# Kernel tuning notes

Hardware: AMD Instinct MI355X
Metric: run time of the kernel (lower is better)

The kernel has to match this reference:

```python
import jax, jax.numpy as jnp
import numpy as np


def setup_inputs() -> dict:
    key = jax.random.key(0)
    k0, k1, k2, k3 = jax.random.split(key, 4)
    B, C, L1, L2, U = 256, 128, 32, 32, 128
    return {
        "inputs": jax.random.normal(k0, (B, C, L1, L2), jnp.float32),
        "W": jax.random.normal(k1, (C + 3 * U, 7 * U), jnp.float32) * 0.05,
        "Umat": jax.random.normal(k2, (3 * U, U), jnp.float32) * 0.05,
        "bias": jnp.zeros((8 * U,), jnp.float32),
        "w_ij": jax.random.normal(k3, (C, U), jnp.float32) * 0.05,
    }


def _hard_sigmoid(x):
    # keras hard_sigmoid
    return jnp.clip(0.2 * x + 0.5, 0.0, 1.0)


def _spatial_gru(inputs, W, Umat, bias, w_ij):
    B, C, L1, L2 = inputs.shape
    U = w_ij.shape[1]
    wr, wz = W[:, : 3 * U], W[:, 3 * U : 7 * U]
    br, bz, b_ij = bias[: 3 * U], bias[3 * U : 7 * U], bias[7 * U :]
    s = jnp.transpose(inputs, (2, 3, 0, 1))  # (L1, L2, B, C)
    h0 = jnp.zeros((B, U), inputs.dtype)

    def cell(h_left, inp):
        h_diag, h_top, s_ij = inp  # each (B, U) / (B, C)
        # q = [h_top, h_left, h_diag, s_ij]  (B, 3U + C)
        q = jnp.concatenate([h_top, h_left, h_diag, s_ij], axis=1)
        r = _hard_sigmoid(q @ wr + br)                      # (B, 3U)
        z = q @ wz + bz                                     # (B, 4U)
        # softmax across the 4 gates per unit (softmax_by_row)
        zg = jax.nn.softmax(z.reshape(B, 4, U), axis=1)
        zi, zl, zt, zd = zg[:, 0], zg[:, 1], zg[:, 2], zg[:, 3]
        hij_ = jnp.tanh(
            s_ij @ w_ij + b_ij
            + (r * jnp.concatenate([h_left, h_top, h_diag], axis=1)) @ Umat
        )
        hij = zl * h_left + zt * h_top + zd * h_diag + zi * hij_
        return hij, hij

    def row(prev_row, s_row):
        # prev_row: (L2+1, B, U) hidden states of row above, boundary h0 at col 0
        # h_diag_j = prev_row[j], h_top_j = prev_row[j+1]
        _, row_h = jax.lax.scan(cell, h0, (prev_row[:-1], prev_row[1:], s_row))
        new_row = jnp.concatenate([h0[None], row_h], axis=0)  # (L2+1, B, U)
        return new_row, None

    init_row = jnp.zeros((L2 + 1, B, U), inputs.dtype)
    last_row, _ = jax.lax.scan(row, init_row, s)
    return last_row[-1]  # h at bottom-right cell, (B, U)


def reference(inputs, W, Umat, bias, w_ij):
    return _spatial_gru(inputs, W, Umat, bias, w_ij)
```

## Files before the change

### kernel.cpp

```cpp
#include <hip/hip_runtime.h>
#include <hip/hip_bf16.h>

typedef _Float16 f16x8 __attribute__((ext_vector_type(8)));
typedef float f32x4 __attribute__((ext_vector_type(4)));

#define BATCH 256
#define UD 128
#define K1 512
#define LDA 520
#define LDA2 392
#define CELLSZ (BATCH*UD)
#define RINGSZ (32*CELLSZ)

__global__ void k_reorder(const float* __restrict__ in, _Float16* __restrict__ X){
  int b = blockIdx.x, i = blockIdx.y;
  __shared__ float tile[128][33];
  int tid = threadIdx.x;
#pragma unroll
  for (int r=0;r<16;++r){
    int c = r*8 + (tid>>5), j = tid&31;
    tile[c][j] = in[(((size_t)b*128 + c)*32 + i)*32 + j];
  }
  __syncthreads();
#pragma unroll
  for (int r=0;r<16;++r){
    int j = r*2 + (tid>>7), c = tid&127;
    X[((size_t)(i*32 + j)*256 + b)*128 + c] = (_Float16)tile[c][j];
  }
}

__global__ void k_prep(const float* __restrict__ W,
                       const float* __restrict__ Um,
                       const float* __restrict__ wij,
                       _Float16* __restrict__ WT, _Float16* __restrict__ B2T){
  int idx = blockIdx.x*256 + threadIdx.x;
  if (idx < 896*512){
    int n = idx >> 9, k = idx & 511;
    WT[idx] = (_Float16)W[k*896 + n];
  }
  if (idx < 128*512){
    int n = idx >> 9, k = idx & 511;
    float v = (k < 384) ? Um[k*128 + n] : wij[(k-384)*128 + n];
    B2T[idx] = (_Float16)v;
  }
}

__global__ void k_out(const float* __restrict__ ring, float* __restrict__ out){
  int t = blockIdx.x*256 + threadIdx.x;
  out[t] = ring[(size_t)2*RINGSZ + (size_t)31*CELLSZ + t];
}

__global__ __launch_bounds__(256, 1) void k_diag(
    int d,
    const _Float16* __restrict__ X,
    float* __restrict__ ring,
    const _Float16* __restrict__ WT,
    const _Float16* __restrict__ B2T,
    const float* __restrict__ bias)
{
  __shared__ __align__(16) _Float16 Al[32*LDA];
  __shared__ __align__(16) _Float16 A2l[32*LDA2];

  const int i0 = (d > 31) ? (d - 31) : 0;
  const int i = i0 + blockIdx.x;
  const int j = d - i;
  const int bs = blockIdx.y * 32;

  const int tid  = threadIdx.x;
  const int wave = tid >> 6;
  const int lane = tid & 63;
  const int l15  = lane & 15;
  const int quad = lane >> 4;

  const bool hasT = (i >= 1);
  const bool hasL = (j >= 1);
  const bool hasD = hasT && hasL;

  const float* rm1 = ring + (size_t)((d+2)%3)*RINGSZ;
  const float* rm2 = ring + (size_t)((d+1)%3)*RINGSZ;
  float*       rw  = ring + (size_t)(d%3)*RINGSZ;

  const float* hTop  = rm1 + (size_t)(i-1)*CELLSZ;
  const float* hLeft = rm1 + (size_t)i*CELLSZ;
  const float* hDiag = rm2 + (size_t)(i-1)*CELLSZ;
  float*       hOut  = rw  + (size_t)i*CELLSZ;
  const _Float16* Xc = X + (size_t)(i*32 + j)*CELLSZ;

  {
    const float* srcs[3];
    srcs[0] = hasT ? hTop : nullptr;
    srcs[1] = hasL ? hLeft : nullptr;
    srcs[2] = hasD ? hDiag : nullptr;
#pragma unroll
    for (int r=0;r<3;++r){
      const float* src = srcs[r];
      if (src){
        for (int v = tid; v < 1024; v += 256){
          int m = v >> 5, kc = (v & 31) << 2;
          float4 f = *(const float4*)(src + (size_t)(bs+m)*UD + kc);
          union { _Float16 h[4]; ushort4 u; } p;
          p.h[0]=(_Float16)f.x; p.h[1]=(_Float16)f.y;
          p.h[2]=(_Float16)f.z; p.h[3]=(_Float16)f.w;
          *(ushort4*)&Al[m*LDA + r*128 + kc] = p.u;
        }
      } else {
        for (int v = tid; v < 1024; v += 256){
          int m = v >> 5, kc = (v & 31) << 2;
          *(ushort4*)&Al[m*LDA + r*128 + kc] = make_ushort4(0,0,0,0);
        }
      }
    }
    for (int v = tid; v < 512; v += 256){
      int m = v >> 4, kc = (v & 15) << 3;
      *(uint4*)&Al[m*LDA + 384 + kc] = *(const uint4*)(Xc + (size_t)(bs+m)*UD + kc);
    }
  }
  __syncthreads();

  f32x4 acc[2][14];
#pragma unroll
  for (int a=0;a<2;++a)
#pragma unroll
    for (int t=0;t<14;++t) acc[a][t] = (f32x4){0.f,0.f,0.f,0.f};

  {
    const _Float16* bptr[14];
#pragma unroll
    for (int t=0;t<14;++t){
      const int n = (t<6) ? (wave*96 + t*16)
                          : (384 + ((t-6)>>1)*128 + wave*32 + ((t-6)&1)*16);
      bptr[t] = WT + (size_t)(n + l15)*K1 + quad*8;
    }
    f16x8 bcur[14], bnxt[14];
#pragma unroll
    for (int t=0;t<14;++t) bcur[t] = *(const f16x8*)(bptr[t]);
#pragma unroll
    for (int ks=0; ks<16; ++ks){
      const int kb = ks*32 + quad*8;
      if (ks < 15){
#pragma unroll
        for (int t=0;t<14;++t) bnxt[t] = *(const f16x8*)(bptr[t] + (ks+1)*32);
      }
      f16x8 a0 = *(const f16x8*)&Al[l15*LDA + kb];
      f16x8 a1 = *(const f16x8*)&Al[(16+l15)*LDA + kb];
#pragma unroll
      for (int t=0;t<14;++t){
        acc[0][t] = __builtin_amdgcn_mfma_f32_16x16x32_f16(a0, bcur[t], acc[0][t], 0,0,0);
        acc[1][t] = __builtin_amdgcn_mfma_f32_16x16x32_f16(a1, bcur[t], acc[1][t], 0,0,0);
      }
#pragma unroll
      for (int t=0;t<14;++t) bcur[t] = bnxt[t];
    }
  }

#pragma unroll
  for (int mt=0;mt<2;++mt)
#pragma unroll
    for (int t=0;t<6;++t){
      const int col = wave*96 + t*16 + l15;
      const float br = bias[col];
      const int hcol = (col < 128) ? (128 + col) : ((col < 256) ? (col - 128) : col);
#pragma unroll
      for (int rg=0;rg<4;++rg){
        const int m = mt*16 + quad*4 + rg;
        float r = 0.2f*(acc[mt][t][rg] + br) + 0.5f;
        r = fminf(fmaxf(r, 0.f), 1.f);
        float h = (float)Al[m*LDA + hcol];
        A2l[m*LDA2 + col] = (_Float16)(r*h);
      }
    }
  __syncthreads();

  f32x4 acc2[2][2];
#pragma unroll
  for (int a=0;a<2;++a){ acc2[a][0]=(f32x4){0.f,0.f,0.f,0.f}; acc2[a][1]=(f32x4){0.f,0.f,0.f,0.f}; }
  {
    const _Float16* b2ptr[2];
#pragma unroll
    for (int s=0;s<2;++s) b2ptr[s] = B2T + (size_t)(wave*32 + s*16 + l15)*K1 + quad*8;
    f16x8 b2cur[2], b2nxt[2];
#pragma unroll
    for (int s=0;s<2;++s) b2cur[s] = *(const f16x8*)(b2ptr[s]);
#pragma unroll
    for (int ks=0; ks<16; ++ks){
      const int kb = ks*32 + quad*8;
      if (ks < 15){
#pragma unroll
        for (int s=0;s<2;++s) b2nxt[s] = *(const f16x8*)(b2ptr[s] + (ks+1)*32);
      }
      f16x8 a0, a1;
      if (ks < 12){
        a0 = *(const f16x8*)&A2l[l15*LDA2 + kb];
        a1 = *(const f16x8*)&A2l[(16+l15)*LDA2 + kb];
      } else {
        a0 = *(const f16x8*)&Al[l15*LDA + kb];
        a1 = *(const f16x8*)&Al[(16+l15)*LDA + kb];
      }
#pragma unroll
      for (int s=0;s<2;++s){
        acc2[0][s] = __builtin_amdgcn_mfma_f32_16x16x32_f16(a0, b2cur[s], acc2[0][s], 0,0,0);
        acc2[1][s] = __builtin_amdgcn_mfma_f32_16x16x32_f16(a1, b2cur[s], acc2[1][s], 0,0,0);
      }
#pragma unroll
      for (int s=0;s<2;++s) b2cur[s] = b2nxt[s];
    }
  }

#pragma unroll
  for (int mt=0;mt<2;++mt)
#pragma unroll
    for (int s=0;s<2;++s){
      const int u = wave*32 + s*16 + l15;
      const float bz0 = bias[384 + 0*128 + u];
      const float bz1 = bias[384 + 1*128 + u];
      const float bz2 = bias[384 + 2*128 + u];
      const float bz3 = bias[384 + 3*128 + u];
      const float bij = bias[896 + u];
#pragma unroll
      for (int rg=0;rg<4;++rg){
        const int m = mt*16 + quad*4 + rg;
        const size_t row = (size_t)(bs+m)*UD + u;
        float z0 = acc[mt][6 + 0 + s][rg] + bz0;
        float z1 = acc[mt][6 + 2 + s][rg] + bz1;
        float z2 = acc[mt][6 + 4 + s][rg] + bz2;
        float z3 = acc[mt][6 + 6 + s][rg] + bz3;
        float mx = fmaxf(fmaxf(z0,z1), fmaxf(z2,z3));
        float e0 = __expf(z0-mx), e1 = __expf(z1-mx), e2 = __expf(z2-mx), e3 = __expf(z3-mx);
        float inv = 1.f/(e0+e1+e2+e3);
        float hl = hasL ? hLeft[row] : 0.f;
        float ht = hasT ? hTop[row]  : 0.f;
        float hd = hasD ? hDiag[row] : 0.f;
        float cand = tanhf(acc2[mt][s][rg] + bij);
        hOut[row] = (e1*hl + e2*ht + e3*hd + e0*cand)*inv;
      }
    }
}

extern "C" void kernel_launch(void* const* d_in, const int* in_sizes, int n_in,
                              void* d_out, int out_size, void* d_ws, size_t ws_size,
                              hipStream_t stream){
  const float* inp  = (const float*)d_in[0];
  const float* W    = (const float*)d_in[1];
  const float* Um   = (const float*)d_in[2];
  const float* bias = (const float*)d_in[3];
  const float* wij  = (const float*)d_in[4];
  float* out = (float*)d_out;

  char* ws = (char*)d_ws;
  _Float16* WT   = (_Float16*)(ws);
  _Float16* B2T  = (_Float16*)(ws + 917504);
  _Float16* X    = (_Float16*)(ws + 1048576);
  float*    ring = (float*)   (ws + 68157440);

  k_reorder<<<dim3(256,32),256,0,stream>>>(inp, X);
  k_prep<<<1792,256,0,stream>>>(W, Um, wij, WT, B2T);
  for (int d=0; d<63; ++d){
    int ilo = (d>31)?(d-31):0, ihi = (d<31)?d:31;
    int nc = ihi - ilo + 1;
    k_diag<<<dim3(nc,8),256,0,stream>>>(d, X, ring, WT, B2T, bias);
  }
  k_out<<<128,256,0,stream>>>(ring, out);
}
```

Before: 2.778 ms.

## Replace per-diagonal launches with persistent wavefront kernel using per-cell flags

```diff
diff --git a/kernel.cpp b/kernel.cpp
--- a/kernel.cpp
+++ b/kernel.cpp
@@ -10,7 +10,11 @@
 #define LDA 520
 #define LDA2 392
 #define CELLSZ (BATCH*UD)
-#define RINGSZ (32*CELLSZ)
+
+#define WS_B2T  917504
+#define WS_X    1048576
+#define WS_H    68157440ull
+#define WS_FLAG 202375168ull
 
 __global__ void k_reorder(const float* __restrict__ in, _Float16* __restrict__ X){
   int b = blockIdx.x, i = blockIdx.y;
@@ -32,7 +36,8 @@
 __global__ void k_prep(const float* __restrict__ W,
                        const float* __restrict__ Um,
                        const float* __restrict__ wij,
-                       _Float16* __restrict__ WT, _Float16* __restrict__ B2T){
+                       _Float16* __restrict__ WT, _Float16* __restrict__ B2T,
+                       unsigned* __restrict__ flags){
   int idx = blockIdx.x*256 + threadIdx.x;
   if (idx < 896*512){
     int n = idx >> 9, k = idx & 511;
@@ -43,28 +48,63 @@
     float v = (k < 384) ? Um[k*128 + n] : wij[(k-384)*128 + n];
     B2T[idx] = (_Float16)v;
   }
-}
-
-__global__ void k_out(const float* __restrict__ ring, float* __restrict__ out){
+  if (idx < 1024*8) flags[idx] = 0;
+}
+
+__global__ void k_out(const float* __restrict__ H, float* __restrict__ out){
   int t = blockIdx.x*256 + threadIdx.x;
-  out[t] = ring[(size_t)2*RINGSZ + (size_t)31*CELLSZ + t];
-}
-
-__global__ __launch_bounds__(256, 1) void k_diag(
-    int d,
+  out[t] = H[(size_t)1023*CELLSZ + t];
+}
+
+template<int T0>
+__device__ __forceinline__ void gemm1_pass(const _Float16* Al,
+    const _Float16* __restrict__ WT, int wave, int l15, int quad,
+    f32x4 (&acc)[2][7])
+{
+  const _Float16* bptr[7];
+#pragma unroll
+  for (int t=0;t<7;++t){
+    const int tt = T0 + t;
+    const int n = (tt<6) ? (wave*96 + tt*16)
+                         : (384 + ((tt-6)>>1)*128 + wave*32 + ((tt-6)&1)*16);
+    bptr[t] = WT + (size_t)(n + l15)*K1 + quad*8;
+  }
+  f16x8 bcur[7], bnxt[7];
+#pragma unroll
+  for (int t=0;t<7;++t) bcur[t] = *(const f16x8*)(bptr[t]);
+#pragma unroll
+  for (int ks=0; ks<16; ++ks){
+    const int kb = ks*32 + quad*8;
+    if (ks < 15){
+#pragma unroll
+      for (int t=0;t<7;++t) bnxt[t] = *(const f16x8*)(bptr[t] + (ks+1)*32);
+    }
+    f16x8 a0 = *(const f16x8*)&Al[l15*LDA + kb];
+    f16x8 a1 = *(const f16x8*)&Al[(16+l15)*LDA + kb];
+#pragma unroll
+    for (int t=0;t<7;++t){
+      acc[0][t] = __builtin_amdgcn_mfma_f32_16x16x32_f16(a0, bcur[t], acc[0][t], 0,0,0);
+      acc[1][t] = __builtin_amdgcn_mfma_f32_16x16x32_f16(a1, bcur[t], acc[1][t], 0,0,0);
+    }
+#pragma unroll
+    for (int t=0;t<7;++t) bcur[t] = bnxt[t];
+  }
+}
+
+__global__ __launch_bounds__(256, 2) void k_sweep(
     const _Float16* __restrict__ X,
-    float* __restrict__ ring,
+    float* __restrict__ H,
     const _Float16* __restrict__ WT,
     const _Float16* __restrict__ B2T,
-    const float* __restrict__ bias)
+    const float* __restrict__ bias,
+    unsigned* __restrict__ flags)
 {
   __shared__ __align__(16) _Float16 Al[32*LDA];
   __shared__ __align__(16) _Float16 A2l[32*LDA2];
 
-  const int i0 = (d > 31) ? (d - 31) : 0;
-  const int i = i0 + blockIdx.x;
-  const int j = d - i;
-  const int bs = blockIdx.y * 32;
+  const int c     = blockIdx.x;
+  const int strip = blockIdx.y;
+  const int bs    = strip*32;
 
   const int tid  = threadIdx.x;
   const int wave = tid >> 6;
@@ -72,168 +112,173 @@
   const int l15  = lane & 15;
   const int quad = lane >> 4;
 
-  const bool hasT = (i >= 1);
-  const bool hasL = (j >= 1);
-  const bool hasD = hasT && hasL;
-
-  const float* rm1 = ring + (size_t)((d+2)%3)*RINGSZ;
-  const float* rm2 = ring + (size_t)((d+1)%3)*RINGSZ;
-  float*       rw  = ring + (size_t)(d%3)*RINGSZ;
-
-  const float* hTop  = rm1 + (size_t)(i-1)*CELLSZ;
-  const float* hLeft = rm1 + (size_t)i*CELLSZ;
-  const float* hDiag = rm2 + (size_t)(i-1)*CELLSZ;
-  float*       hOut  = rw  + (size_t)i*CELLSZ;
-  const _Float16* Xc = X + (size_t)(i*32 + j)*CELLSZ;
-
-  {
-    const float* srcs[3];
-    srcs[0] = hasT ? hTop : nullptr;
-    srcs[1] = hasL ? hLeft : nullptr;
-    srcs[2] = hasD ? hDiag : nullptr;
-#pragma unroll
-    for (int r=0;r<3;++r){
-      const float* src = srcs[r];
-      if (src){
-        for (int v = tid; v < 1024; v += 256){
-          int m = v >> 5, kc = (v & 31) << 2;
-          float4 f = *(const float4*)(src + (size_t)(bs+m)*UD + kc);
-          union { _Float16 h[4]; ushort4 u; } p;
-          p.h[0]=(_Float16)f.x; p.h[1]=(_Float16)f.y;
-          p.h[2]=(_Float16)f.z; p.h[3]=(_Float16)f.w;
-          *(ushort4*)&Al[m*LDA + r*128 + kc] = p.u;
-        }
-      } else {
-        for (int v = tid; v < 1024; v += 256){
-          int m = v >> 5, kc = (v & 31) << 2;
-          *(ushort4*)&Al[m*LDA + r*128 + kc] = make_ushort4(0,0,0,0);
-        }
-      }
-    }
+  for (int d = c; d <= 62 - c; ++d){
+    const int i0 = (d > 31) ? (d - 31) : 0;
+    const int i  = i0 + c;
+    const int j  = d - i;
+    const bool hasT = (i >= 1);
+    const bool hasL = (j >= 1);
+    const bool hasD = hasT && hasL;
+
+    const int cell = i*32 + j;
+    const _Float16* Xc   = X + (size_t)cell*CELLSZ;
+    float*       hOut    = H + (size_t)cell*CELLSZ;
+    const float* hTop    = H + (size_t)(cell-32)*CELLSZ;
+    const float* hLeft   = H + (size_t)(cell-1)*CELLSZ;
+    const float* hDiag   = H + (size_t)(cell-33)*CELLSZ;
+
     for (int v = tid; v < 512; v += 256){
       int m = v >> 4, kc = (v & 15) << 3;
       *(uint4*)&Al[m*LDA + 384 + kc] = *(const uint4*)(Xc + (size_t)(bs+m)*UD + kc);
     }
-  }
-  __syncthreads();
-
-  f32x4 acc[2][14];
-#pragma unroll
-  for (int a=0;a<2;++a)
-#pragma unroll
-    for (int t=0;t<14;++t) acc[a][t] = (f32x4){0.f,0.f,0.f,0.f};
-
-  {
-    const _Float16* bptr[14];
-#pragma unroll
-    for (int t=0;t<14;++t){
-      const int n = (t<6) ? (wave*96 + t*16)
-                          : (384 + ((t-6)>>1)*128 + wave*32 + ((t-6)&1)*16);
-      bptr[t] = WT + (size_t)(n + l15)*K1 + quad*8;
-    }
-    f16x8 bcur[14], bnxt[14];
-#pragma unroll
-    for (int t=0;t<14;++t) bcur[t] = *(const f16x8*)(bptr[t]);
-#pragma unroll
-    for (int ks=0; ks<16; ++ks){
-      const int kb = ks*32 + quad*8;
-      if (ks < 15){
-#pragma unroll
-        for (int t=0;t<14;++t) bnxt[t] = *(const f16x8*)(bptr[t] + (ks+1)*32);
-      }
-      f16x8 a0 = *(const f16x8*)&Al[l15*LDA + kb];
-      f16x8 a1 = *(const f16x8*)&Al[(16+l15)*LDA + kb];
-#pragma unroll
-      for (int t=0;t<14;++t){
-        acc[0][t] = __builtin_amdgcn_mfma_f32_16x16x32_f16(a0, bcur[t], acc[0][t], 0,0,0);
-        acc[1][t] = __builtin_amdgcn_mfma_f32_16x16x32_f16(a1, bcur[t], acc[1][t], 0,0,0);
-      }
-#pragma unroll
-      for (int t=0;t<14;++t) bcur[t] = bnxt[t];
-    }
-  }
-
-#pragma unroll
-  for (int mt=0;mt<2;++mt)
-#pragma unroll
-    for (int t=0;t<6;++t){
-      const int col = wave*96 + t*16 + l15;
-      const float br = bias[col];
-      const int hcol = (col < 128) ? (128 + col) : ((col < 256) ? (col - 128) : col);
-#pragma unroll
-      for (int rg=0;rg<4;++rg){
-        const int m = mt*16 + quad*4 + rg;
-        float r = 0.2f*(acc[mt][t][rg] + br) + 0.5f;
-        r = fminf(fmaxf(r, 0.f), 1.f);
-        float h = (float)Al[m*LDA + hcol];
-        A2l[m*LDA2 + col] = (_Float16)(r*h);
-      }
-    }
-  __syncthreads();
-
-  f32x4 acc2[2][2];
-#pragma unroll
-  for (int a=0;a<2;++a){ acc2[a][0]=(f32x4){0.f,0.f,0.f,0.f}; acc2[a][1]=(f32x4){0.f,0.f,0.f,0.f}; }
-  {
-    const _Float16* b2ptr[2];
-#pragma unroll
-    for (int s=0;s<2;++s) b2ptr[s] = B2T + (size_t)(wave*32 + s*16 + l15)*K1 + quad*8;
-    f16x8 b2cur[2], b2nxt[2];
-#pragma unroll
-    for (int s=0;s<2;++s) b2cur[s] = *(const f16x8*)(b2ptr[s]);
-#pragma unroll
-    for (int ks=0; ks<16; ++ks){
-      const int kb = ks*32 + quad*8;
-      if (ks < 15){
-#pragma unroll
-        for (int s=0;s<2;++s) b2nxt[s] = *(const f16x8*)(b2ptr[s] + (ks+1)*32);
-      }
-      f16x8 a0, a1;
-      if (ks < 12){
-        a0 = *(const f16x8*)&A2l[l15*LDA2 + kb];
-        a1 = *(const f16x8*)&A2l[(16+l15)*LDA2 + kb];
-      } else {
-        a0 = *(const f16x8*)&Al[l15*LDA + kb];
-        a1 = *(const f16x8*)&Al[(16+l15)*LDA + kb];
-      }
+    if (!hasT || !hasL){
+#pragma unroll
+      for (int r=0;r<3;++r){
+        const bool present = (r==0) ? hasT : ((r==1) ? hasL : hasD);
+        if (!present){
+          for (int v = tid; v < 1024; v += 256){
+            int m = v >> 5, kc = (v & 31) << 2;
+            *(ushort4*)&Al[m*LDA + r*128 + kc] = make_ushort4(0,0,0,0);
+          }
+        }
+      }
+    }
+
+    if (tid < 3){
+      const unsigned* f = nullptr;
+      if (tid==0 && hasT) f = &flags[(size_t)(cell-32)*8 + strip];
+      if (tid==1 && hasL) f = &flags[(size_t)(cell-1)*8 + strip];
+      if (tid==2 && hasD) f = &flags[(size_t)(cell-33)*8 + strip];
+      if (f){
+        while (__hip_atomic_load(f, __ATOMIC_RELAXED, __HIP_MEMORY_SCOPE_AGENT) == 0)
+          __builtin_amdgcn_s_sleep(1);
+      }
+    }
+    __syncthreads();
+
+    {
+      const float* srcs[3];
+      srcs[0] = hasT ? hTop : nullptr;
+      srcs[1] = hasL ? hLeft : nullptr;
+      srcs[2] = hasD ? hDiag : nullptr;
+#pragma unroll
+      for (int r=0;r<3;++r){
+        const float* src = srcs[r];
+        if (src){
+          for (int v = tid; v < 1024; v += 256){
+            int m = v >> 5, kc = (v & 31) << 2;
+            float4 f4 = *(const float4*)(src + (size_t)(bs+m)*UD + kc);
+            union { _Float16 h[4]; ushort4 u; } p;
+            p.h[0]=(_Float16)f4.x; p.h[1]=(_Float16)f4.y;
+            p.h[2]=(_Float16)f4.z; p.h[3]=(_Float16)f4.w;
+            *(ushort4*)&Al[m*LDA + r*128 + kc] = p.u;
+          }
+        }
+      }
+    }
+    __syncthreads();
+
+    f32x4 accA[2][7];
+#pragma unroll
+    for (int a=0;a<2;++a)
+#pragma unroll
+      for (int t=0;t<7;++t) accA[a][t] = (f32x4){0.f,0.f,0.f,0.f};
+    gemm1_pass<0>(Al, WT, wave, l15, quad, accA);
+
+#pragma unroll
+    for (int mt=0;mt<2;++mt)
+#pragma unroll
+      for (int t=0;t<6;++t){
+        const int col = wave*96 + t*16 + l15;
+        const float br = bias[col];
+        const int hcol = (col < 128) ? (128 + col) : ((col < 256) ? (col - 128) : col);
+#pragma unroll
+        for (int rg=0;rg<4;++rg){
+          const int m = mt*16 + quad*4 + rg;
+          float r = 0.2f*(accA[mt][t][rg] + br) + 0.5f;
+          r = fminf(fmaxf(r, 0.f), 1.f);
+          float h = (float)Al[m*LDA + hcol];
+          A2l[m*LDA2 + col] = (_Float16)(r*h);
+        }
+      }
+
+    f32x4 accB[2][7];
+#pragma unroll
+    for (int a=0;a<2;++a)
+#pragma unroll
+      for (int t=0;t<7;++t) accB[a][t] = (f32x4){0.f,0.f,0.f,0.f};
+    gemm1_pass<7>(Al, WT, wave, l15, quad, accB);
+    __syncthreads();
+
+    f32x4 acc2[2][2];
+#pragma unroll
+    for (int a=0;a<2;++a){ acc2[a][0]=(f32x4){0.f,0.f,0.f,0.f}; acc2[a][1]=(f32x4){0.f,0.f,0.f,0.f}; }
+    {
+      const _Float16* b2ptr[2];
+#pragma unroll
+      for (int s=0;s<2;++s) b2ptr[s] = B2T + (size_t)(wave*32 + s*16 + l15)*K1 + quad*8;
+      f16x8 b2cur[2], b2nxt[2];
+#pragma unroll
+      for (int s=0;s<2;++s) b2cur[s] = *(const f16x8*)(b2ptr[s]);
+#pragma unroll
+      for (int ks=0; ks<16; ++ks){
+        const int kb = ks*32 + quad*8;
+        if (ks < 15){
+#pragma unroll
+          for (int s=0;s<2;++s) b2nxt[s] = *(const f16x8*)(b2ptr[s] + (ks+1)*32);
+        }
+        f16x8 a0, a1;
+        if (ks < 12){
+          a0 = *(const f16x8*)&A2l[l15*LDA2 + kb];
+          a1 = *(const f16x8*)&A2l[(16+l15)*LDA2 + kb];
+        } else {
+          a0 = *(const f16x8*)&Al[l15*LDA + kb];
+          a1 = *(const f16x8*)&Al[(16+l15)*LDA + kb];
+        }
+#pragma unroll
+        for (int s=0;s<2;++s){
+          acc2[0][s] = __builtin_amdgcn_mfma_f32_16x16x32_f16(a0, b2cur[s], acc2[0][s], 0,0,0);
+          acc2[1][s] = __builtin_amdgcn_mfma_f32_16x16x32_f16(a1, b2cur[s], acc2[1][s], 0,0,0);
+        }
+#pragma unroll
+        for (int s=0;s<2;++s) b2cur[s] = b2nxt[s];
+      }
+    }
+
+#pragma unroll
+    for (int mt=0;mt<2;++mt)
 #pragma unroll
       for (int s=0;s<2;++s){
-        acc2[0][s] = __builtin_amdgcn_mfma_f32_16x16x32_f16(a0, b2cur[s], acc2[0][s], 0,0,0);
-        acc2[1][s] = __builtin_amdgcn_mfma_f32_16x16x32_f16(a1, b2cur[s], acc2[1][s], 0,0,0);
-      }
-#pragma unroll
-      for (int s=0;s<2;++s) b2cur[s] = b2nxt[s];
-    }
-  }
-
-#pragma unroll
-  for (int mt=0;mt<2;++mt)
-#pragma unroll
-    for (int s=0;s<2;++s){
-      const int u = wave*32 + s*16 + l15;
-      const float bz0 = bias[384 + 0*128 + u];
-      const float bz1 = bias[384 + 1*128 + u];
-      const float bz2 = bias[384 + 2*128 + u];
-      const float bz3 = bias[384 + 3*128 + u];
-      const float bij = bias[896 + u];
-#pragma unroll
-      for (int rg=0;rg<4;++rg){
-        const int m = mt*16 + quad*4 + rg;
-        const size_t row = (size_t)(bs+m)*UD + u;
-        float z0 = acc[mt][6 + 0 + s][rg] + bz0;
-        float z1 = acc[mt][6 + 2 + s][rg] + bz1;
-        float z2 = acc[mt][6 + 4 + s][rg] + bz2;
-        float z3 = acc[mt][6 + 6 + s][rg] + bz3;
-        float mx = fmaxf(fmaxf(z0,z1), fmaxf(z2,z3));
-        float e0 = __expf(z0-mx), e1 = __expf(z1-mx), e2 = __expf(z2-mx), e3 = __expf(z3-mx);
-        float inv = 1.f/(e0+e1+e2+e3);
-        float hl = hasL ? hLeft[row] : 0.f;
-        float ht = hasT ? hTop[row]  : 0.f;
-        float hd = hasD ? hDiag[row] : 0.f;
-        float cand = tanhf(acc2[mt][s][rg] + bij);
-        hOut[row] = (e1*hl + e2*ht + e3*hd + e0*cand)*inv;
-      }
-    }
+        const int u = wave*32 + s*16 + l15;
+        const float bz0 = bias[384 + u];
+        const float bz1 = bias[512 + u];
+        const float bz2 = bias[640 + u];
+        const float bz3 = bias[768 + u];
+        const float bij = bias[896 + u];
+#pragma unroll
+        for (int rg=0;rg<4;++rg){
+          const int m = mt*16 + quad*4 + rg;
+          const size_t row = (size_t)(bs+m)*UD + u;
+          float z0 = ((s==0) ? accA[mt][6][rg] : accB[mt][0][rg]) + bz0;
+          float z1 = accB[mt][1+s][rg] + bz1;
+          float z2 = accB[mt][3+s][rg] + bz2;
+          float z3 = accB[mt][5+s][rg] + bz3;
+          float mx = fmaxf(fmaxf(z0,z1), fmaxf(z2,z3));
+          float e0 = __expf(z0-mx), e1 = __expf(z1-mx), e2 = __expf(z2-mx), e3 = __expf(z3-mx);
+          float inv = 1.f/(e0+e1+e2+e3);
+          float hl = hasL ? hLeft[row] : 0.f;
+          float ht = hasT ? hTop[row]  : 0.f;
+          float hd = hasD ? hDiag[row] : 0.f;
+          float cand = tanhf(acc2[mt][s][rg] + bij);
+          hOut[row] = (e1*hl + e2*ht + e3*hd + e0*cand)*inv;
+        }
+      }
+
+    __syncthreads();
+    if (tid == 0)
+      __hip_atomic_store(&flags[(size_t)cell*8 + strip], 1u,
+                         __ATOMIC_RELEASE, __HIP_MEMORY_SCOPE_AGENT);
+  }
 }
 
 extern "C" void kernel_launch(void* const* d_in, const int* in_sizes, int n_in,
@@ -247,17 +292,14 @@
   float* out = (float*)d_out;
 
   char* ws = (char*)d_ws;
-  _Float16* WT   = (_Float16*)(ws);
-  _Float16* B2T  = (_Float16*)(ws + 917504);
-  _Float16* X    = (_Float16*)(ws + 1048576);
-  float*    ring = (float*)   (ws + 68157440);
+  _Float16* WT    = (_Float16*)(ws);
+  _Float16* B2T   = (_Float16*)(ws + WS_B2T);
+  _Float16* X     = (_Float16*)(ws + WS_X);
+  float*    H     = (float*)   (ws + WS_H);
+  unsigned* flags = (unsigned*)(ws + WS_FLAG);
 
   k_reorder<<<dim3(256,32),256,0,stream>>>(inp, X);
-  k_prep<<<1792,256,0,stream>>>(W, Um, wij, WT, B2T);
-  for (int d=0; d<63; ++d){
-    int ilo = (d>31)?(d-31):0, ihi = (d<31)?d:31;
-    int nc = ihi - ilo + 1;
-    k_diag<<<dim3(nc,8),256,0,stream>>>(d, X, ring, WT, B2T, bias);
-  }
-  k_out<<<128,256,0,stream>>>(ring, out);
-}
+  k_prep<<<1792,256,0,stream>>>(W, Um, wij, WT, B2T, flags);
+  k_sweep<<<dim3(32,8),256,0,stream>>>(X, H, WT, B2T, bias, flags);
+  k_out<<<128,256,0,stream>>>(H, out);
+}
```

Result: slower. 5.713 ms (+105.7%).
